# Performance work log

Hardware: AMD Instinct MI355X
Metric: run time of the kernel (lower is better)

The kernel has to match this reference:

```python
import jax, jax.numpy as jnp
import numpy as np
from jax import lax

ALPHA = 5.0   # ATan surrogate alpha
TAU = 2.0     # LIF tau
HEADS = 16
SCALE = 0.25

@jax.custom_vjp
def atan_spike(x):
    return (x >= 0.0).astype(x.dtype)

def _atan_fwd(x):
    return atan_spike(x), x

def _atan_bwd(x, g):
    # spikingjelly surrogate.ATan: d/dx = alpha/2 / (1 + (pi/2*alpha*x)^2)
    return (g * (ALPHA / 2.0) / (1.0 + (jnp.pi / 2.0 * ALPHA * x) ** 2),)

atan_spike.defvjp(_atan_fwd, _atan_bwd)

def lif(x, v_th=1.0):
    # Multi-step LIF, hard reset to 0, detach_reset=True. x: [T, ...]
    def step(v, xt):
        h = v + (xt - v) / TAU
        s = atan_spike(h - v_th)
        v_new = h * (1.0 - lax.stop_gradient(s))
        return v_new, s
    _, spikes = lax.scan(step, jnp.zeros_like(x[0]), x)
    return spikes

def conv_bn(x, w, gamma, beta, mean, var, eps=1e-5):
    # 1x1 Conv1d (bias=False) + BatchNorm1d (eval stats). x: [..., C, N]
    y = jnp.einsum('oc,...cn->...on', w, x)
    scale = gamma * lax.rsqrt(var + eps)
    return y * scale[:, None] + (beta - mean * scale)[:, None]

def setup_inputs() -> dict:
    key = jax.random.key(0)
    ks = jax.random.split(key, 22)
    T, B, C, H, W = 4, 8, 256, 32, 16
    d = {}
    d['x'] = jax.random.normal(ks[0], (T, B, C, H, W), jnp.float32)
    i = 1
    for n in ['q', 'k', 'v', 'proj']:
        d[n + '_w'] = jax.random.normal(ks[i], (C, C), jnp.float32) / 16.0; i += 1
        d[n + '_gamma'] = jax.random.uniform(ks[i], (C,), jnp.float32, 0.5, 1.5); i += 1
        d[n + '_beta'] = jax.random.normal(ks[i], (C,), jnp.float32) * 0.1; i += 1
        d[n + '_mean'] = jax.random.normal(ks[i], (C,), jnp.float32) * 0.1; i += 1
        d[n + '_var'] = jax.random.uniform(ks[i], (C,), jnp.float32, 0.5, 1.5); i += 1
    return d

def reference(x, q_w, q_gamma, q_beta, q_mean, q_var,
              k_w, k_gamma, k_beta, k_mean, k_var,
              v_w, v_gamma, v_beta, v_mean, v_var,
              proj_w, proj_gamma, proj_beta, proj_mean, proj_var):
    T, B, C, H, W = x.shape
    N = H * W
    hd = C // HEADS
    xf = x.reshape(T, B, C, N)

    def branch(w, g, b, m, v):
        s = lif(conv_bn(xf, w, g, b, m, v))  # [T,B,C,N] binary spikes
        # -> [T,B,heads,N,head_dim]
        return s.transpose(0, 1, 3, 2).reshape(T, B, N, HEADS, hd).transpose(0, 1, 3, 2, 4)

    q = branch(q_w, q_gamma, q_beta, q_mean, q_var)
    k = branch(k_w, k_gamma, k_beta, k_mean, k_var)
    v = branch(v_w, v_gamma, v_beta, v_mean, v_var)

    attn = jnp.einsum('tbhnd,tbhmd->tbhnm', q, k)           # binary q@k^T
    y = jnp.einsum('tbhnm,tbhmd->tbhnd', attn, v) * SCALE   # (attn @ v) * 0.25
    y = y.transpose(0, 1, 2, 4, 3).reshape(T, B, C, N)       # transpose(3,4) then merge heads

    # attn_lif is applied on flatten(0,1): time dim = T*B (faithful to source)
    s = lif(y.reshape(T * B, C, N), v_th=0.5)
    p = conv_bn(s, proj_w, proj_gamma, proj_beta, proj_mean, proj_var)
    out = lif(p.reshape(T, B, C, W, H))  # note W,H swap, as in source
    return out
```

## Files before the change

kernel.cpp:

```cpp
#include <hip/hip_runtime.h>

#define TT 4
#define BB 8
#define CC 256
#define NN 512
#define HEADS 16
#define HD 16

#define GLL16(gp, lp) \
    __builtin_amdgcn_global_load_lds( \
        (const __attribute__((address_space(1))) void*)(gp), \
        (__attribute__((address_space(3))) void*)(lp), 16, 0, 0)

struct WPtrs  { const float* w[4]; };
struct BnPtrs { const float* g[4]; const float* b[4]; const float* m[4]; const float* v[4]; };

__global__ __launch_bounds__(256)
void prep_bn(BnPtrs p, float* __restrict__ sc, float* __restrict__ bi)
{
    int m = blockIdx.x, c = threadIdx.x;
    float rs = __fdiv_rn(1.0f, __fsqrt_rn(__fadd_rn(p.v[m][c], 1e-5f)));
    float s  = __fmul_rn(p.g[m][c], rs);
    sc[m * CC + c] = s;
    bi[m * CC + c] = __fsub_rn(p.b[m][c], __fmul_rn(p.m[m][c], s));
}

__global__ __launch_bounds__(256)
void transpose_w(WPtrs p, float* __restrict__ wt)
{
    __shared__ float t[16][17];
    const int m  = blockIdx.z;
    const float* w = p.w[m];
    const int o0 = blockIdx.y * 16, k0 = blockIdx.x * 16;
    const int tx = threadIdx.x, ty = threadIdx.y;
    t[ty][tx] = w[(size_t)(o0 + ty) * CC + k0 + tx];
    __syncthreads();
    wt[(size_t)m * CC * CC + (size_t)(k0 + ty) * CC + o0 + tx] = t[tx][ty];
}

__global__ __launch_bounds__(256, 4)
void qkv_conv_bn_lif_pack(const float* __restrict__ x,
                          const float* __restrict__ wt,
                          const float* __restrict__ scA,
                          const float* __restrict__ biA,
                          unsigned long long* __restrict__ bits)
{
    __shared__ float W2[2][32][64];
    __shared__ float X2[2][32][64];
    __shared__ unsigned short Spk[64][16];

    const int tid = threadIdx.x;
    const int tx = tid & 15;
    const int ty = tid >> 4;
    const int br = blockIdx.z >> 3;
    const int b  = blockIdx.z & 7;
    const int o0 = blockIdx.y * 64;
    const int n0 = blockIdx.x * 64;

    const float* wtb = wt + (size_t)br * CC * CC;
    unsigned long long* bout = bits + (size_t)br * (TT * BB * CC * 8);

    float sc[4], bi[4];
#pragma unroll
    for (int i = 0; i < 4; ++i) {
        sc[i] = scA[br * CC + o0 + ty * 4 + i];
        bi[i] = biA[br * CC + o0 + ty * 4 + i];
    }

    auto stage = [&](int s, int buf) {
        const int t  = s >> 3;
        const int k0 = (s & 7) * 32;
        const float* xb = x + (size_t)(t * BB + b) * CC * NN;
#pragma unroll
        for (int i = 0; i < 2; ++i) {
            int idx = tid + 256 * i;
            int row = idx >> 4;
            int cg  = idx & 15;
            GLL16(&wtb[(size_t)(k0 + row) * CC + o0 + cg * 4], &W2[buf][row][cg * 4]);
            GLL16(&xb [(size_t)(k0 + row) * NN + n0 + cg * 4], &X2[buf][row][cg * 4]);
        }
    };

    float vst[4][4];
    float acc[4][4];
    unsigned int tnib[4] = {0u, 0u, 0u, 0u};
#pragma unroll
    for (int i = 0; i < 4; ++i)
#pragma unroll
        for (int j = 0; j < 4; ++j) { vst[i][j] = 0.0f; acc[i][j] = 0.0f; }

    stage(0, 0);
    __syncthreads();

    int cur = 0;
    for (int s = 0; s < 32; ++s) {
        if (s < 31) stage(s + 1, cur ^ 1);

#pragma unroll 8
        for (int kk = 0; kk < 32; ++kk) {
            float4 wv = *reinterpret_cast<const float4*>(&W2[cur][kk][ty * 4]);
            float4 xv = *reinterpret_cast<const float4*>(&X2[cur][kk][tx * 4]);
#pragma unroll
            for (int i = 0; i < 4; ++i) {
                float wvi = (i == 0) ? wv.x : (i == 1) ? wv.y : (i == 2) ? wv.z : wv.w;
                acc[i][0] = __fmaf_rn(wvi, xv.x, acc[i][0]);
                acc[i][1] = __fmaf_rn(wvi, xv.y, acc[i][1]);
                acc[i][2] = __fmaf_rn(wvi, xv.z, acc[i][2]);
                acc[i][3] = __fmaf_rn(wvi, xv.w, acc[i][3]);
            }
        }

        if ((s & 7) == 7) {
            const int t = s >> 3;
#pragma unroll
            for (int i = 0; i < 4; ++i) {
                unsigned int nib = 0u;
#pragma unroll
                for (int j = 0; j < 4; ++j) {
                    float ybn = __fadd_rn(__fmul_rn(acc[i][j], sc[i]), bi[i]);
                    float h   = __fadd_rn(vst[i][j],
                                          __fmul_rn(__fsub_rn(ybn, vst[i][j]), 0.5f));
                    bool sp = (h >= 1.0f);
                    vst[i][j] = sp ? 0.0f : h;
                    nib |= (sp ? 1u : 0u) << j;
                    acc[i][j] = 0.0f;
                }
                tnib[i] |= nib << (4 * t);
            }
        }

        __syncthreads();
        cur ^= 1;
    }

#pragma unroll
    for (int i = 0; i < 4; ++i) Spk[ty * 4 + i][tx] = (unsigned short)tnib[i];
    __syncthreads();
    if (tid < 64) {
#pragma unroll
        for (int t = 0; t < 4; ++t) {
            unsigned long long m = 0ULL;
#pragma unroll
            for (int g = 0; g < 16; ++g)
                m |= (unsigned long long)((Spk[tid][g] >> (4 * t)) & 0xF) << (4 * g);
            bout[((size_t)(t * BB + b) * CC + o0 + tid) * 8 + blockIdx.x] = m;
        }
    }
}

__global__ __launch_bounds__(256)
void attn_kernel(const unsigned long long* __restrict__ bq,
                 const unsigned long long* __restrict__ bk,
                 const unsigned long long* __restrict__ bv,
                 float* __restrict__ y)
{
    const int blk = blockIdx.x;
    const int h  = blk & 15;
    const int tb = blk >> 4;
    const int tid = threadIdx.x;

    __shared__ unsigned long long kb[16][8], vb[16][8], qb[16][8];
    __shared__ float M[16][16];

    size_t base = ((size_t)tb * CC + h * HD) * 8;
    if (tid < 128) {
        int j = tid >> 3, ch = tid & 7;
        kb[j][ch] = bk[base + j * 8 + ch];
        vb[j][ch] = bv[base + j * 8 + ch];
        qb[j][ch] = bq[base + j * 8 + ch];
    }
    __syncthreads();

    {
        int j = tid >> 4, d = tid & 15;
        int cnt = 0;
#pragma unroll
        for (int ch = 0; ch < 8; ++ch)
            cnt += __popcll(kb[j][ch] & vb[d][ch]);
        M[j][d] = (float)cnt;
    }
    __syncthreads();

    size_t ybase = ((size_t)tb * CC + h * HD) * (size_t)NN;
#pragma unroll
    for (int r = 0; r < 2; ++r) {
        int n = tid + 256 * r;
        int ch = n >> 6, sh = n & 63;
        float acc[16];
#pragma unroll
        for (int d = 0; d < 16; ++d) acc[d] = 0.0f;
#pragma unroll
        for (int j = 0; j < 16; ++j) {
            float bit = (float)((qb[j][ch] >> sh) & 1ULL);
#pragma unroll
            for (int d = 0; d < 16; ++d)
                acc[d] = __fmaf_rn(bit, M[j][d], acc[d]);
        }
#pragma unroll
        for (int d = 0; d < 16; ++d)
            y[ybase + (size_t)d * NN + n] = __fmul_rn(acc[d], 0.25f);
    }
}

__global__ __launch_bounds__(256)
void attn_lif(float* __restrict__ y)
{
    const int e = blockIdx.x * 256 + threadIdx.x;
    float xs[32];
#pragma unroll
    for (int tb = 0; tb < 32; ++tb)
        xs[tb] = y[(size_t)tb * (CC * NN) + e];
    float v = 0.0f;
#pragma unroll
    for (int tb = 0; tb < 32; ++tb) {
        float h = __fadd_rn(v, __fmul_rn(__fsub_rn(xs[tb], v), 0.5f));
        bool sp = (h >= 0.5f);
        y[(size_t)tb * (CC * NN) + e] = sp ? 1.0f : 0.0f;
        v = sp ? 0.0f : h;
    }
}

__global__ __launch_bounds__(256, 4)
void proj_bn_lif(const float* __restrict__ sfl,
                 const float* __restrict__ wt,
                 const float* __restrict__ scA,
                 const float* __restrict__ biA,
                 float* __restrict__ out)
{
    __shared__ float W2[2][32][64];
    __shared__ float X2[2][32][32];

    const int tid = threadIdx.x;
    const int tx = tid & 15;
    const int ty = tid >> 4;
    const int b  = blockIdx.z;
    const int o0 = blockIdx.y * 64;
    const int n0 = blockIdx.x * 32;

    float sc[4], bi[4];
#pragma unroll
    for (int i = 0; i < 4; ++i) {
        sc[i] = scA[3 * CC + o0 + ty * 4 + i];
        bi[i] = biA[3 * CC + o0 + ty * 4 + i];
    }

    auto stage = [&](int s, int buf) {
        const int t  = s >> 3;
        const int k0 = (s & 7) * 32;
        const float* sb = sfl + (size_t)(t * BB + b) * CC * NN;
#pragma unroll
        for (int i = 0; i < 2; ++i) {
            int idx = tid + 256 * i;
            int row = idx >> 4, cg = idx & 15;
            GLL16(&wt[(size_t)(k0 + row) * CC + o0 + cg * 4], &W2[buf][row][cg * 4]);
        }
        {
            int row = tid >> 3, cg = tid & 7;
            GLL16(&sb[(size_t)(k0 + row) * NN + n0 + cg * 4], &X2[buf][row][cg * 4]);
        }
    };

    float vst[4][2], acc[4][2];
#pragma unroll
    for (int i = 0; i < 4; ++i) {
        vst[i][0] = 0.0f; vst[i][1] = 0.0f;
        acc[i][0] = 0.0f; acc[i][1] = 0.0f;
    }

    stage(0, 0);
    __syncthreads();

    int cur = 0;
    for (int s = 0; s < 32; ++s) {
        if (s < 31) stage(s + 1, cur ^ 1);

#pragma unroll 8
        for (int kk = 0; kk < 32; ++kk) {
            float4 wv = *reinterpret_cast<const float4*>(&W2[cur][kk][ty * 4]);
            float2 xv = *reinterpret_cast<const float2*>(&X2[cur][kk][tx * 2]);
#pragma unroll
            for (int i = 0; i < 4; ++i) {
                float wvi = (i == 0) ? wv.x : (i == 1) ? wv.y : (i == 2) ? wv.z : wv.w;
                acc[i][0] = __fmaf_rn(wvi, xv.x, acc[i][0]);
                acc[i][1] = __fmaf_rn(wvi, xv.y, acc[i][1]);
            }
        }

        if ((s & 7) == 7) {
            const int t = s >> 3;
#pragma unroll
            for (int i = 0; i < 4; ++i) {
                float2 o2;
                float r[2];
#pragma unroll
                for (int j = 0; j < 2; ++j) {
                    float ybn = __fadd_rn(__fmul_rn(acc[i][j], sc[i]), bi[i]);
                    float h   = __fadd_rn(vst[i][j],
                                          __fmul_rn(__fsub_rn(ybn, vst[i][j]), 0.5f));
                    bool sp = (h >= 1.0f);
                    vst[i][j] = sp ? 0.0f : h;
                    r[j] = sp ? 1.0f : 0.0f;
                    acc[i][j] = 0.0f;
                }
                o2.x = r[0]; o2.y = r[1];
                *reinterpret_cast<float2*>(
                    &out[((size_t)(t * BB + b) * CC + o0 + ty * 4 + i) * NN + n0 + tx * 2]) = o2;
            }
        }

        __syncthreads();
        cur ^= 1;
    }
}

extern "C" void kernel_launch(void* const* d_in, const int* in_sizes, int n_in,
                              void* d_out, int out_size, void* d_ws, size_t ws_size,
                              hipStream_t stream) {
    const float* x = (const float*)d_in[0];

    WPtrs wp;
    BnPtrs bp;
    for (int m = 0; m < 4; ++m) {
        wp.w[m] = (const float*)d_in[1 + m * 5 + 0];
        bp.g[m] = (const float*)d_in[1 + m * 5 + 1];
        bp.b[m] = (const float*)d_in[1 + m * 5 + 2];
        bp.m[m] = (const float*)d_in[1 + m * 5 + 3];
        bp.v[m] = (const float*)d_in[1 + m * 5 + 4];
    }

    char* ws = (char*)d_ws;
    float* wt   = (float*)ws;
    float* scA  = (float*)(ws + (1u << 20));
    float* biA  = (float*)(ws + (1u << 20) + 4096);
    unsigned long long* bits = (unsigned long long*)(ws + (1u << 20) + 8192);
    float* ybuf = (float*)(ws + (1u << 20) + 8192 + (1536u << 10));

    prep_bn<<<4, 256, 0, stream>>>(bp, scA, biA);
    transpose_w<<<dim3(16, 16, 4), dim3(16, 16), 0, stream>>>(wp, wt);

    qkv_conv_bn_lif_pack<<<dim3(8, 4, 24), 256, 0, stream>>>(x, wt, scA, biA, bits);

    const unsigned long long* bq = bits;
    const unsigned long long* bk = bits + 65536;
    const unsigned long long* bv = bits + 131072;
    attn_kernel<<<512, 256, 0, stream>>>(bq, bk, bv, ybuf);
    attn_lif<<<512, 256, 0, stream>>>(ybuf);
    proj_bn_lif<<<dim3(16, 4, 8), 256, 0, stream>>>(ybuf, wt + 3 * CC * CC, scA, biA, (float*)d_out);
}
```

Before: 266.8 us.

## Fuse Q/K/V conv branches per block and read weights as wave-uniform scalars

```diff
diff --git a/kernel.cpp b/kernel.cpp
--- a/kernel.cpp
+++ b/kernel.cpp
@@ -38,56 +38,56 @@
     wt[(size_t)m * CC * CC + (size_t)(k0 + ty) * CC + o0 + tx] = t[tx][ty];
 }
 
-__global__ __launch_bounds__(256, 4)
+__global__ __launch_bounds__(256)
 void qkv_conv_bn_lif_pack(const float* __restrict__ x,
                           const float* __restrict__ wt,
                           const float* __restrict__ scA,
                           const float* __restrict__ biA,
                           unsigned long long* __restrict__ bits)
 {
-    __shared__ float W2[2][32][64];
-    __shared__ float X2[2][32][64];
-    __shared__ unsigned short Spk[64][16];
-
-    const int tid = threadIdx.x;
-    const int tx = tid & 15;
-    const int ty = tid >> 4;
-    const int br = blockIdx.z >> 3;
-    const int b  = blockIdx.z & 7;
-    const int o0 = blockIdx.y * 64;
-    const int n0 = blockIdx.x * 64;
-
-    const float* wtb = wt + (size_t)br * CC * CC;
-    unsigned long long* bout = bits + (size_t)br * (TT * BB * CC * 8);
-
-    float sc[4], bi[4];
-#pragma unroll
-    for (int i = 0; i < 4; ++i) {
-        sc[i] = scA[br * CC + o0 + ty * 4 + i];
-        bi[i] = biA[br * CC + o0 + ty * 4 + i];
-    }
+    __shared__ float X2[2][32 * 128];
+
+    const int tid  = threadIdx.x;
+    const int lane = tid & 63;
+    const int wv   = __builtin_amdgcn_readfirstlane(tid >> 6);
+    const int b  = blockIdx.z;
+    const int o0 = blockIdx.y * 32;
+    const int n0 = blockIdx.x * 128;
+    const int wo0 = o0 + wv * 8;
+
+    const float* w0 = wt + (size_t)0 * CC * CC + wo0;
+    const float* w1 = wt + (size_t)1 * CC * CC + wo0;
+    const float* w2 = wt + (size_t)2 * CC * CC + wo0;
+
+    float sc[3][8], bi[3][8];
+#pragma unroll
+    for (int m = 0; m < 3; ++m)
+#pragma unroll
+        for (int o = 0; o < 8; ++o) {
+            sc[m][o] = scA[m * CC + wo0 + o];
+            bi[m][o] = biA[m * CC + wo0 + o];
+        }
 
     auto stage = [&](int s, int buf) {
         const int t  = s >> 3;
         const int k0 = (s & 7) * 32;
-        const float* xb = x + (size_t)(t * BB + b) * CC * NN;
-#pragma unroll
-        for (int i = 0; i < 2; ++i) {
+        const float* xb = x + (size_t)(t * BB + b) * (CC * NN);
+#pragma unroll
+        for (int i = 0; i < 4; ++i) {
             int idx = tid + 256 * i;
-            int row = idx >> 4;
-            int cg  = idx & 15;
-            GLL16(&wtb[(size_t)(k0 + row) * CC + o0 + cg * 4], &W2[buf][row][cg * 4]);
-            GLL16(&xb [(size_t)(k0 + row) * NN + n0 + cg * 4], &X2[buf][row][cg * 4]);
+            GLL16(&xb[(size_t)(k0 + (idx >> 5)) * NN + n0 + (idx & 31) * 4],
+                  &X2[buf][idx * 4]);
         }
     };
 
-    float vst[4][4];
-    float acc[4][4];
-    unsigned int tnib[4] = {0u, 0u, 0u, 0u};
-#pragma unroll
-    for (int i = 0; i < 4; ++i)
-#pragma unroll
-        for (int j = 0; j < 4; ++j) { vst[i][j] = 0.0f; acc[i][j] = 0.0f; }
+    float acc[3][8][2], vst[3][8][2];
+#pragma unroll
+    for (int m = 0; m < 3; ++m)
+#pragma unroll
+        for (int o = 0; o < 8; ++o) {
+            acc[m][o][0] = 0.0f; acc[m][o][1] = 0.0f;
+            vst[m][o][0] = 0.0f; vst[m][o][1] = 0.0f;
+        }
 
     stage(0, 0);
     __syncthreads();
@@ -96,55 +96,67 @@
     for (int s = 0; s < 32; ++s) {
         if (s < 31) stage(s + 1, cur ^ 1);
 
-#pragma unroll 8
+        const int k0 = (s & 7) * 32;
+        const float* Xc = &X2[cur][0];
+        const float* wr0 = w0 + (size_t)k0 * CC;
+        const float* wr1 = w1 + (size_t)k0 * CC;
+        const float* wr2 = w2 + (size_t)k0 * CC;
+
+#pragma unroll
         for (int kk = 0; kk < 32; ++kk) {
-            float4 wv = *reinterpret_cast<const float4*>(&W2[cur][kk][ty * 4]);
-            float4 xv = *reinterpret_cast<const float4*>(&X2[cur][kk][tx * 4]);
-#pragma unroll
-            for (int i = 0; i < 4; ++i) {
-                float wvi = (i == 0) ? wv.x : (i == 1) ? wv.y : (i == 2) ? wv.z : wv.w;
-                acc[i][0] = __fmaf_rn(wvi, xv.x, acc[i][0]);
-                acc[i][1] = __fmaf_rn(wvi, xv.y, acc[i][1]);
-                acc[i][2] = __fmaf_rn(wvi, xv.z, acc[i][2]);
-                acc[i][3] = __fmaf_rn(wvi, xv.w, acc[i][3]);
+            float x0 = Xc[kk * 128 + lane];
+            float x1 = Xc[kk * 128 + 64 + lane];
+#pragma unroll
+            for (int o = 0; o < 8; ++o) {
+                float a0 = wr0[kk * CC + o];
+                float a1 = wr1[kk * CC + o];
+                float a2 = wr2[kk * CC + o];
+                acc[0][o][0] = __fmaf_rn(a0, x0, acc[0][o][0]);
+                acc[0][o][1] = __fmaf_rn(a0, x1, acc[0][o][1]);
+                acc[1][o][0] = __fmaf_rn(a1, x0, acc[1][o][0]);
+                acc[1][o][1] = __fmaf_rn(a1, x1, acc[1][o][1]);
+                acc[2][o][0] = __fmaf_rn(a2, x0, acc[2][o][0]);
+                acc[2][o][1] = __fmaf_rn(a2, x1, acc[2][o][1]);
             }
         }
 
         if ((s & 7) == 7) {
             const int t = s >> 3;
 #pragma unroll
-            for (int i = 0; i < 4; ++i) {
-                unsigned int nib = 0u;
-#pragma unroll
-                for (int j = 0; j < 4; ++j) {
-                    float ybn = __fadd_rn(__fmul_rn(acc[i][j], sc[i]), bi[i]);
-                    float h   = __fadd_rn(vst[i][j],
-                                          __fmul_rn(__fsub_rn(ybn, vst[i][j]), 0.5f));
-                    bool sp = (h >= 1.0f);
-                    vst[i][j] = sp ? 0.0f : h;
-                    nib |= (sp ? 1u : 0u) << j;
-                    acc[i][j] = 0.0f;
+            for (int m = 0; m < 3; ++m) {
+                unsigned long long* bout = bits + (size_t)m * (TT * BB * CC * 8);
+#pragma unroll
+                for (int o = 0; o < 8; ++o) {
+                    unsigned long long msk0, msk1;
+                    {
+                        float ybn = __fadd_rn(__fmul_rn(acc[m][o][0], sc[m][o]), bi[m][o]);
+                        float h   = __fadd_rn(vst[m][o][0],
+                                              __fmul_rn(__fsub_rn(ybn, vst[m][o][0]), 0.5f));
+                        bool sp = (h >= 1.0f);
+                        vst[m][o][0] = sp ? 0.0f : h;
+                        msk0 = __ballot(sp ? 1 : 0);
+                        acc[m][o][0] = 0.0f;
+                    }
+                    {
+                        float ybn = __fadd_rn(__fmul_rn(acc[m][o][1], sc[m][o]), bi[m][o]);
+                        float h   = __fadd_rn(vst[m][o][1],
+                                              __fmul_rn(__fsub_rn(ybn, vst[m][o][1]), 0.5f));
+                        bool sp = (h >= 1.0f);
+                        vst[m][o][1] = sp ? 0.0f : h;
+                        msk1 = __ballot(sp ? 1 : 0);
+                        acc[m][o][1] = 0.0f;
+                    }
+                    if (lane == 0) {
+                        size_t bo = ((size_t)(t * BB + b) * CC + wo0 + o) * 8 + (n0 >> 6);
+                        bout[bo + 0] = msk0;
+                        bout[bo + 1] = msk1;
+                    }
                 }
-                tnib[i] |= nib << (4 * t);
             }
         }
 
         __syncthreads();
         cur ^= 1;
-    }
-
-#pragma unroll
-    for (int i = 0; i < 4; ++i) Spk[ty * 4 + i][tx] = (unsigned short)tnib[i];
-    __syncthreads();
-    if (tid < 64) {
-#pragma unroll
-        for (int t = 0; t < 4; ++t) {
-            unsigned long long m = 0ULL;
-#pragma unroll
-            for (int g = 0; g < 16; ++g)
-                m |= (unsigned long long)((Spk[tid][g] >> (4 * t)) & 0xF) << (4 * g);
-            bout[((size_t)(t * BB + b) * CC + o0 + tid) * 8 + blockIdx.x] = m;
-        }
     }
 }
 
@@ -220,51 +232,49 @@
     }
 }
 
-__global__ __launch_bounds__(256, 4)
+__global__ __launch_bounds__(256)
 void proj_bn_lif(const float* __restrict__ sfl,
-                 const float* __restrict__ wt,
+                 const float* __restrict__ wt3,
                  const float* __restrict__ scA,
                  const float* __restrict__ biA,
                  float* __restrict__ out)
 {
-    __shared__ float W2[2][32][64];
-    __shared__ float X2[2][32][32];
-
-    const int tid = threadIdx.x;
-    const int tx = tid & 15;
-    const int ty = tid >> 4;
+    __shared__ float X2[2][32 * 128];
+
+    const int tid  = threadIdx.x;
+    const int lane = tid & 63;
+    const int wv   = __builtin_amdgcn_readfirstlane(tid >> 6);
     const int b  = blockIdx.z;
-    const int o0 = blockIdx.y * 64;
-    const int n0 = blockIdx.x * 32;
-
-    float sc[4], bi[4];
-#pragma unroll
-    for (int i = 0; i < 4; ++i) {
-        sc[i] = scA[3 * CC + o0 + ty * 4 + i];
-        bi[i] = biA[3 * CC + o0 + ty * 4 + i];
+    const int o0 = blockIdx.y * 32;
+    const int n0 = blockIdx.x * 128;
+    const int wo0 = o0 + wv * 8;
+
+    const float* w0 = wt3 + wo0;
+
+    float sc[8], bi[8];
+#pragma unroll
+    for (int o = 0; o < 8; ++o) {
+        sc[o] = scA[3 * CC + wo0 + o];
+        bi[o] = biA[3 * CC + wo0 + o];
     }
 
     auto stage = [&](int s, int buf) {
         const int t  = s >> 3;
         const int k0 = (s & 7) * 32;
-        const float* sb = sfl + (size_t)(t * BB + b) * CC * NN;
-#pragma unroll
-        for (int i = 0; i < 2; ++i) {
+        const float* xb = sfl + (size_t)(t * BB + b) * (CC * NN);
+#pragma unroll
+        for (int i = 0; i < 4; ++i) {
             int idx = tid + 256 * i;
-            int row = idx >> 4, cg = idx & 15;
-            GLL16(&wt[(size_t)(k0 + row) * CC + o0 + cg * 4], &W2[buf][row][cg * 4]);
-        }
-        {
-            int row = tid >> 3, cg = tid & 7;
-            GLL16(&sb[(size_t)(k0 + row) * NN + n0 + cg * 4], &X2[buf][row][cg * 4]);
+            GLL16(&xb[(size_t)(k0 + (idx >> 5)) * NN + n0 + (idx & 31) * 4],
+                  &X2[buf][idx * 4]);
         }
     };
 
-    float vst[4][2], acc[4][2];
-#pragma unroll
-    for (int i = 0; i < 4; ++i) {
-        vst[i][0] = 0.0f; vst[i][1] = 0.0f;
-        acc[i][0] = 0.0f; acc[i][1] = 0.0f;
+    float acc[8][2], vst[8][2];
+#pragma unroll
+    for (int o = 0; o < 8; ++o) {
+        acc[o][0] = 0.0f; acc[o][1] = 0.0f;
+        vst[o][0] = 0.0f; vst[o][1] = 0.0f;
     }
 
     stage(0, 0);
@@ -274,37 +284,37 @@
     for (int s = 0; s < 32; ++s) {
         if (s < 31) stage(s + 1, cur ^ 1);
 
-#pragma unroll 8
+        const int k0 = (s & 7) * 32;
+        const float* Xc = &X2[cur][0];
+        const float* wr = w0 + (size_t)k0 * CC;
+
+#pragma unroll
         for (int kk = 0; kk < 32; ++kk) {
-            float4 wv = *reinterpret_cast<const float4*>(&W2[cur][kk][ty * 4]);
-            float2 xv = *reinterpret_cast<const float2*>(&X2[cur][kk][tx * 2]);
-#pragma unroll
-            for (int i = 0; i < 4; ++i) {
-                float wvi = (i == 0) ? wv.x : (i == 1) ? wv.y : (i == 2) ? wv.z : wv.w;
-                acc[i][0] = __fmaf_rn(wvi, xv.x, acc[i][0]);
-                acc[i][1] = __fmaf_rn(wvi, xv.y, acc[i][1]);
+            float x0 = Xc[kk * 128 + lane];
+            float x1 = Xc[kk * 128 + 64 + lane];
+#pragma unroll
+            for (int o = 0; o < 8; ++o) {
+                float a = wr[kk * CC + o];
+                acc[o][0] = __fmaf_rn(a, x0, acc[o][0]);
+                acc[o][1] = __fmaf_rn(a, x1, acc[o][1]);
             }
         }
 
         if ((s & 7) == 7) {
             const int t = s >> 3;
 #pragma unroll
-            for (int i = 0; i < 4; ++i) {
-                float2 o2;
-                float r[2];
+            for (int o = 0; o < 8; ++o) {
 #pragma unroll
                 for (int j = 0; j < 2; ++j) {
-                    float ybn = __fadd_rn(__fmul_rn(acc[i][j], sc[i]), bi[i]);
-                    float h   = __fadd_rn(vst[i][j],
-                                          __fmul_rn(__fsub_rn(ybn, vst[i][j]), 0.5f));
+                    float ybn = __fadd_rn(__fmul_rn(acc[o][j], sc[o]), bi[o]);
+                    float h   = __fadd_rn(vst[o][j],
+                                          __fmul_rn(__fsub_rn(ybn, vst[o][j]), 0.5f));
                     bool sp = (h >= 1.0f);
-                    vst[i][j] = sp ? 0.0f : h;
-                    r[j] = sp ? 1.0f : 0.0f;
-                    acc[i][j] = 0.0f;
+                    vst[o][j] = sp ? 0.0f : h;
+                    acc[o][j] = 0.0f;
+                    out[((size_t)(t * BB + b) * CC + wo0 + o) * NN + n0 + j * 64 + lane]
+                        = sp ? 1.0f : 0.0f;
                 }
-                o2.x = r[0]; o2.y = r[1];
-                *reinterpret_cast<float2*>(
-                    &out[((size_t)(t * BB + b) * CC + o0 + ty * 4 + i) * NN + n0 + tx * 2]) = o2;
             }
         }
 
@@ -338,12 +348,12 @@
     prep_bn<<<4, 256, 0, stream>>>(bp, scA, biA);
     transpose_w<<<dim3(16, 16, 4), dim3(16, 16), 0, stream>>>(wp, wt);
 
-    qkv_conv_bn_lif_pack<<<dim3(8, 4, 24), 256, 0, stream>>>(x, wt, scA, biA, bits);
+    qkv_conv_bn_lif_pack<<<dim3(4, 8, 8), 256, 0, stream>>>(x, wt, scA, biA, bits);
 
     const unsigned long long* bq = bits;
     const unsigned long long* bk = bits + 65536;
     const unsigned long long* bv = bits + 131072;
     attn_kernel<<<512, 256, 0, stream>>>(bq, bk, bv, ybuf);
     attn_lif<<<512, 256, 0, stream>>>(ybuf);
-    proj_bn_lif<<<dim3(16, 4, 8), 256, 0, stream>>>(ybuf, wt + 3 * CC * CC, scA, biA, (float*)d_out);
-}
+    proj_bn_lif<<<dim3(4, 8, 8), 256, 0, stream>>>(ybuf, wt + 3 * CC * CC, scA, biA, (float*)d_out);
+}
```

Measured after the change: 789.3 us. +195.9%, slower.

## Use 128x128 register tiles for QKV GEMM and split proj GEMM from LIF

Applied to the files above, without the earlier changes.

```diff
diff --git a/kernel.cpp b/kernel.cpp
--- a/kernel.cpp
+++ b/kernel.cpp
@@ -38,56 +38,58 @@
     wt[(size_t)m * CC * CC + (size_t)(k0 + ty) * CC + o0 + tx] = t[tx][ty];
 }
 
-__global__ __launch_bounds__(256, 4)
+__global__ __launch_bounds__(256)
 void qkv_conv_bn_lif_pack(const float* __restrict__ x,
                           const float* __restrict__ wt,
                           const float* __restrict__ scA,
                           const float* __restrict__ biA,
                           unsigned long long* __restrict__ bits)
 {
-    __shared__ float W2[2][32][64];
-    __shared__ float X2[2][32][64];
-    __shared__ unsigned short Spk[64][16];
+    __shared__ float Wl[2][32][128];
+    __shared__ float Xl[2][32][128];
+    __shared__ unsigned char Spk[128][16];
 
     const int tid = threadIdx.x;
     const int tx = tid & 15;
     const int ty = tid >> 4;
     const int br = blockIdx.z >> 3;
     const int b  = blockIdx.z & 7;
-    const int o0 = blockIdx.y * 64;
-    const int n0 = blockIdx.x * 64;
-
-    const float* wtb = wt + (size_t)br * CC * CC;
+    const int o0 = blockIdx.y * 128;
+    const int n0 = blockIdx.x * 128;
+
+    const float* wb = wt + (size_t)br * CC * CC;
     unsigned long long* bout = bits + (size_t)br * (TT * BB * CC * 8);
 
-    float sc[4], bi[4];
-#pragma unroll
-    for (int i = 0; i < 4; ++i) {
-        sc[i] = scA[br * CC + o0 + ty * 4 + i];
-        bi[i] = biA[br * CC + o0 + ty * 4 + i];
+    float sc[8], bi[8];
+#pragma unroll
+    for (int i = 0; i < 8; ++i) {
+        sc[i] = scA[br * CC + o0 + ty * 8 + i];
+        bi[i] = biA[br * CC + o0 + ty * 8 + i];
     }
 
     auto stage = [&](int s, int buf) {
         const int t  = s >> 3;
         const int k0 = (s & 7) * 32;
-        const float* xb = x + (size_t)(t * BB + b) * CC * NN;
-#pragma unroll
-        for (int i = 0; i < 2; ++i) {
+        const float* xb = x + (size_t)(t * BB + b) * (CC * NN);
+#pragma unroll
+        for (int i = 0; i < 4; ++i) {
             int idx = tid + 256 * i;
-            int row = idx >> 4;
-            int cg  = idx & 15;
-            GLL16(&wtb[(size_t)(k0 + row) * CC + o0 + cg * 4], &W2[buf][row][cg * 4]);
-            GLL16(&xb [(size_t)(k0 + row) * NN + n0 + cg * 4], &X2[buf][row][cg * 4]);
+            int row = idx >> 5, cg = idx & 31;
+            GLL16(&wb[(size_t)(k0 + row) * CC + o0 + cg * 4], &Wl[buf][row][cg * 4]);
+        }
+#pragma unroll
+        for (int i = 0; i < 4; ++i) {
+            int idx = tid + 256 * i;
+            int row = idx >> 5, cg = idx & 31;
+            GLL16(&xb[(size_t)(k0 + row) * NN + n0 + cg * 4], &Xl[buf][row][cg * 4]);
         }
     };
 
-    float vst[4][4];
-    float acc[4][4];
-    unsigned int tnib[4] = {0u, 0u, 0u, 0u};
-#pragma unroll
-    for (int i = 0; i < 4; ++i)
-#pragma unroll
-        for (int j = 0; j < 4; ++j) { vst[i][j] = 0.0f; acc[i][j] = 0.0f; }
+    float acc[8][8], vst[8][8];
+#pragma unroll
+    for (int i = 0; i < 8; ++i)
+#pragma unroll
+        for (int j = 0; j < 8; ++j) { acc[i][j] = 0.0f; vst[i][j] = 0.0f; }
 
     stage(0, 0);
     __syncthreads();
@@ -98,53 +100,47 @@
 
 #pragma unroll 8
         for (int kk = 0; kk < 32; ++kk) {
-            float4 wv = *reinterpret_cast<const float4*>(&W2[cur][kk][ty * 4]);
-            float4 xv = *reinterpret_cast<const float4*>(&X2[cur][kk][tx * 4]);
-#pragma unroll
-            for (int i = 0; i < 4; ++i) {
-                float wvi = (i == 0) ? wv.x : (i == 1) ? wv.y : (i == 2) ? wv.z : wv.w;
-                acc[i][0] = __fmaf_rn(wvi, xv.x, acc[i][0]);
-                acc[i][1] = __fmaf_rn(wvi, xv.y, acc[i][1]);
-                acc[i][2] = __fmaf_rn(wvi, xv.z, acc[i][2]);
-                acc[i][3] = __fmaf_rn(wvi, xv.w, acc[i][3]);
-            }
+            const float4 w0 = *reinterpret_cast<const float4*>(&Wl[cur][kk][ty * 8]);
+            const float4 w1 = *reinterpret_cast<const float4*>(&Wl[cur][kk][ty * 8 + 4]);
+            const float4 x0 = *reinterpret_cast<const float4*>(&Xl[cur][kk][tx * 8]);
+            const float4 x1 = *reinterpret_cast<const float4*>(&Xl[cur][kk][tx * 8 + 4]);
+            const float wa[8] = {w0.x, w0.y, w0.z, w0.w, w1.x, w1.y, w1.z, w1.w};
+            const float xa[8] = {x0.x, x0.y, x0.z, x0.w, x1.x, x1.y, x1.z, x1.w};
+#pragma unroll
+            for (int i = 0; i < 8; ++i)
+#pragma unroll
+                for (int j = 0; j < 8; ++j)
+                    acc[i][j] = __fmaf_rn(wa[i], xa[j], acc[i][j]);
         }
 
         if ((s & 7) == 7) {
             const int t = s >> 3;
 #pragma unroll
-            for (int i = 0; i < 4; ++i) {
-                unsigned int nib = 0u;
-#pragma unroll
-                for (int j = 0; j < 4; ++j) {
+            for (int i = 0; i < 8; ++i) {
+                unsigned int byte = 0u;
+#pragma unroll
+                for (int j = 0; j < 8; ++j) {
                     float ybn = __fadd_rn(__fmul_rn(acc[i][j], sc[i]), bi[i]);
                     float h   = __fadd_rn(vst[i][j],
                                           __fmul_rn(__fsub_rn(ybn, vst[i][j]), 0.5f));
                     bool sp = (h >= 1.0f);
                     vst[i][j] = sp ? 0.0f : h;
-                    nib |= (sp ? 1u : 0u) << j;
+                    byte |= (sp ? 1u : 0u) << j;
                     acc[i][j] = 0.0f;
                 }
-                tnib[i] |= nib << (4 * t);
+                Spk[ty * 8 + i][tx] = (unsigned char)byte;
+            }
+            __syncthreads();
+            {
+                int o = tid >> 1, ch = tid & 1;
+                unsigned long long m =
+                    *reinterpret_cast<const unsigned long long*>(&Spk[o][ch * 8]);
+                bout[((size_t)(t * BB + b) * CC + o0 + o) * 8 + (blockIdx.x * 2 + ch)] = m;
             }
         }
 
         __syncthreads();
         cur ^= 1;
-    }
-
-#pragma unroll
-    for (int i = 0; i < 4; ++i) Spk[ty * 4 + i][tx] = (unsigned short)tnib[i];
-    __syncthreads();
-    if (tid < 64) {
-#pragma unroll
-        for (int t = 0; t < 4; ++t) {
-            unsigned long long m = 0ULL;
-#pragma unroll
-            for (int g = 0; g < 16; ++g)
-                m |= (unsigned long long)((Spk[tid][g] >> (4 * t)) & 0xF) << (4 * g);
-            bout[((size_t)(t * BB + b) * CC + o0 + tid) * 8 + blockIdx.x] = m;
-        }
     }
 }
 
@@ -220,96 +216,115 @@
     }
 }
 
-__global__ __launch_bounds__(256, 4)
-void proj_bn_lif(const float* __restrict__ sfl,
-                 const float* __restrict__ wt,
-                 const float* __restrict__ scA,
-                 const float* __restrict__ biA,
-                 float* __restrict__ out)
-{
-    __shared__ float W2[2][32][64];
-    __shared__ float X2[2][32][32];
+__global__ __launch_bounds__(256)
+void proj_gemm_bn(const float* __restrict__ X,
+                  const float* __restrict__ wtp,
+                  const float* __restrict__ scP,
+                  const float* __restrict__ biP,
+                  float* __restrict__ Y)
+{
+    __shared__ float Wl[2][32][128];
+    __shared__ float Xl[2][32][128];
 
     const int tid = threadIdx.x;
     const int tx = tid & 15;
     const int ty = tid >> 4;
-    const int b  = blockIdx.z;
-    const int o0 = blockIdx.y * 64;
-    const int n0 = blockIdx.x * 32;
-
-    float sc[4], bi[4];
-#pragma unroll
-    for (int i = 0; i < 4; ++i) {
-        sc[i] = scA[3 * CC + o0 + ty * 4 + i];
-        bi[i] = biA[3 * CC + o0 + ty * 4 + i];
+    const int tb = blockIdx.z;
+    const int o0 = blockIdx.y * 128;
+    const int n0 = blockIdx.x * 128;
+
+    const float* xb = X + (size_t)tb * (CC * NN);
+
+    float sc[8], bi[8];
+#pragma unroll
+    for (int i = 0; i < 8; ++i) {
+        sc[i] = scP[o0 + ty * 8 + i];
+        bi[i] = biP[o0 + ty * 8 + i];
     }
 
     auto stage = [&](int s, int buf) {
-        const int t  = s >> 3;
-        const int k0 = (s & 7) * 32;
-        const float* sb = sfl + (size_t)(t * BB + b) * CC * NN;
-#pragma unroll
-        for (int i = 0; i < 2; ++i) {
+        const int k0 = s * 32;
+#pragma unroll
+        for (int i = 0; i < 4; ++i) {
             int idx = tid + 256 * i;
-            int row = idx >> 4, cg = idx & 15;
-            GLL16(&wt[(size_t)(k0 + row) * CC + o0 + cg * 4], &W2[buf][row][cg * 4]);
-        }
-        {
-            int row = tid >> 3, cg = tid & 7;
-            GLL16(&sb[(size_t)(k0 + row) * NN + n0 + cg * 4], &X2[buf][row][cg * 4]);
+            int row = idx >> 5, cg = idx & 31;
+            GLL16(&wtp[(size_t)(k0 + row) * CC + o0 + cg * 4], &Wl[buf][row][cg * 4]);
+        }
+#pragma unroll
+        for (int i = 0; i < 4; ++i) {
+            int idx = tid + 256 * i;
+            int row = idx >> 5, cg = idx & 31;
+            GLL16(&xb[(size_t)(k0 + row) * NN + n0 + cg * 4], &Xl[buf][row][cg * 4]);
         }
     };
 
-    float vst[4][2], acc[4][2];
-#pragma unroll
-    for (int i = 0; i < 4; ++i) {
-        vst[i][0] = 0.0f; vst[i][1] = 0.0f;
-        acc[i][0] = 0.0f; acc[i][1] = 0.0f;
-    }
+    float acc[8][8];
+#pragma unroll
+    for (int i = 0; i < 8; ++i)
+#pragma unroll
+        for (int j = 0; j < 8; ++j) acc[i][j] = 0.0f;
 
     stage(0, 0);
     __syncthreads();
 
     int cur = 0;
-    for (int s = 0; s < 32; ++s) {
-        if (s < 31) stage(s + 1, cur ^ 1);
+    for (int s = 0; s < 8; ++s) {
+        if (s < 7) stage(s + 1, cur ^ 1);
 
 #pragma unroll 8
         for (int kk = 0; kk < 32; ++kk) {
-            float4 wv = *reinterpret_cast<const float4*>(&W2[cur][kk][ty * 4]);
-            float2 xv = *reinterpret_cast<const float2*>(&X2[cur][kk][tx * 2]);
-#pragma unroll
-            for (int i = 0; i < 4; ++i) {
-                float wvi = (i == 0) ? wv.x : (i == 1) ? wv.y : (i == 2) ? wv.z : wv.w;
-                acc[i][0] = __fmaf_rn(wvi, xv.x, acc[i][0]);
-                acc[i][1] = __fmaf_rn(wvi, xv.y, acc[i][1]);
-            }
-        }
-
-        if ((s & 7) == 7) {
-            const int t = s >> 3;
-#pragma unroll
-            for (int i = 0; i < 4; ++i) {
-                float2 o2;
-                float r[2];
-#pragma unroll
-                for (int j = 0; j < 2; ++j) {
-                    float ybn = __fadd_rn(__fmul_rn(acc[i][j], sc[i]), bi[i]);
-                    float h   = __fadd_rn(vst[i][j],
-                                          __fmul_rn(__fsub_rn(ybn, vst[i][j]), 0.5f));
-                    bool sp = (h >= 1.0f);
-                    vst[i][j] = sp ? 0.0f : h;
-                    r[j] = sp ? 1.0f : 0.0f;
-                    acc[i][j] = 0.0f;
-                }
-                o2.x = r[0]; o2.y = r[1];
-                *reinterpret_cast<float2*>(
-                    &out[((size_t)(t * BB + b) * CC + o0 + ty * 4 + i) * NN + n0 + tx * 2]) = o2;
-            }
+            const float4 w0 = *reinterpret_cast<const float4*>(&Wl[cur][kk][ty * 8]);
+            const float4 w1 = *reinterpret_cast<const float4*>(&Wl[cur][kk][ty * 8 + 4]);
+            const float4 x0 = *reinterpret_cast<const float4*>(&Xl[cur][kk][tx * 8]);
+            const float4 x1 = *reinterpret_cast<const float4*>(&Xl[cur][kk][tx * 8 + 4]);
+            const float wa[8] = {w0.x, w0.y, w0.z, w0.w, w1.x, w1.y, w1.z, w1.w};
+            const float xa[8] = {x0.x, x0.y, x0.z, x0.w, x1.x, x1.y, x1.z, x1.w};
+#pragma unroll
+            for (int i = 0; i < 8; ++i)
+#pragma unroll
+                for (int j = 0; j < 8; ++j)
+                    acc[i][j] = __fmaf_rn(wa[i], xa[j], acc[i][j]);
         }
 
         __syncthreads();
         cur ^= 1;
+    }
+
+    float* Yp = Y + (size_t)tb * (CC * NN);
+#pragma unroll
+    for (int i = 0; i < 8; ++i) {
+        float r[8];
+#pragma unroll
+        for (int j = 0; j < 8; ++j)
+            r[j] = __fadd_rn(__fmul_rn(acc[i][j], sc[i]), bi[i]);
+        float4 r0 = make_float4(r[0], r[1], r[2], r[3]);
+        float4 r1 = make_float4(r[4], r[5], r[6], r[7]);
+        float* dst = &Yp[(size_t)(o0 + ty * 8 + i) * NN + n0 + tx * 8];
+        *reinterpret_cast<float4*>(dst) = r0;
+        *reinterpret_cast<float4*>(dst + 4) = r1;
+    }
+}
+
+__global__ __launch_bounds__(256)
+void final_lif(const float* __restrict__ Yp, float* __restrict__ out)
+{
+    const size_t stride = (size_t)BB * CC * NN;
+    const int i4 = blockIdx.x * 256 + threadIdx.x;
+    float4 v = make_float4(0.f, 0.f, 0.f, 0.f);
+#pragma unroll
+    for (int t = 0; t < 4; ++t) {
+        float4 xv = *reinterpret_cast<const float4*>(&Yp[t * stride + (size_t)i4 * 4]);
+        float4 o4;
+        float h;
+        h = __fadd_rn(v.x, __fmul_rn(__fsub_rn(xv.x, v.x), 0.5f));
+        o4.x = (h >= 1.0f) ? 1.0f : 0.0f; v.x = (h >= 1.0f) ? 0.0f : h;
+        h = __fadd_rn(v.y, __fmul_rn(__fsub_rn(xv.y, v.y), 0.5f));
+        o4.y = (h >= 1.0f) ? 1.0f : 0.0f; v.y = (h >= 1.0f) ? 0.0f : h;
+        h = __fadd_rn(v.z, __fmul_rn(__fsub_rn(xv.z, v.z), 0.5f));
+        o4.z = (h >= 1.0f) ? 1.0f : 0.0f; v.z = (h >= 1.0f) ? 0.0f : h;
+        h = __fadd_rn(v.w, __fmul_rn(__fsub_rn(xv.w, v.w), 0.5f));
+        o4.w = (h >= 1.0f) ? 1.0f : 0.0f; v.w = (h >= 1.0f) ? 0.0f : h;
+        *reinterpret_cast<float4*>(&out[t * stride + (size_t)i4 * 4]) = o4;
     }
 }
 
@@ -333,17 +348,21 @@
     float* scA  = (float*)(ws + (1u << 20));
     float* biA  = (float*)(ws + (1u << 20) + 4096);
     unsigned long long* bits = (unsigned long long*)(ws + (1u << 20) + 8192);
-    float* ybuf = (float*)(ws + (1u << 20) + 8192 + (1536u << 10));
+    float* ybuf  = (float*)(ws + (1u << 20) + 8192 + 1572864);
+    float* ybn_p = (float*)(ws + (1u << 20) + 8192 + 1572864 + 16777216);
 
     prep_bn<<<4, 256, 0, stream>>>(bp, scA, biA);
     transpose_w<<<dim3(16, 16, 4), dim3(16, 16), 0, stream>>>(wp, wt);
 
-    qkv_conv_bn_lif_pack<<<dim3(8, 4, 24), 256, 0, stream>>>(x, wt, scA, biA, bits);
+    qkv_conv_bn_lif_pack<<<dim3(4, 2, 24), 256, 0, stream>>>(x, wt, scA, biA, bits);
 
     const unsigned long long* bq = bits;
     const unsigned long long* bk = bits + 65536;
     const unsigned long long* bv = bits + 131072;
     attn_kernel<<<512, 256, 0, stream>>>(bq, bk, bv, ybuf);
     attn_lif<<<512, 256, 0, stream>>>(ybuf);
-    proj_bn_lif<<<dim3(16, 4, 8), 256, 0, stream>>>(ybuf, wt + 3 * CC * CC, scA, biA, (float*)d_out);
-}
+
+    proj_gemm_bn<<<dim3(4, 2, 32), 256, 0, stream>>>(
+        ybuf, wt + 3 * CC * CC, scA + 3 * CC, biA + 3 * CC, ybn_p);
+    final_lif<<<1024, 256, 0, stream>>>(ybn_p, (float*)d_out);
+}
```

Result: slower. 297.3 us (+11.5%).
